# Kernel optimization log

Measured on AMD Instinct MI355X. Metric: run time of the kernel, lower is better.

The kernel has to match this reference:

```python
import jax, jax.numpy as jnp
import numpy as np

MASKING_RATIO = 0.5
EPS = 1e-6

def setup_inputs() -> dict:
    key = jax.random.key(0)
    x = jax.random.normal(key, (64, 256, 56, 56), dtype=jnp.float32)
    return {"x": x}

def reference(x):
    B, C, H, W = x.shape
    x_flat = x.reshape(B, C, H * W)
    # stable softmax over spatial dim, + eps as in the original
    probs = jax.nn.softmax(x_flat, axis=-1) + EPS
    entropy = -jnp.sum(probs * jnp.log(probs), axis=-1)  # [B, C]
    importance = -entropy
    k = int(C * (1.0 - MASKING_RATIO))
    _, topk_idx = jax.lax.top_k(importance, k)  # [B, k]
    mask = jnp.zeros((B, C), dtype=x.dtype)
    mask = mask.at[jnp.arange(B)[:, None], topk_idx].set(1.0)
    return x * mask[:, :, None, None]
```

## Files before the change

### kernel.cpp

```cpp
#include <hip/hip_runtime.h>
#include <math.h>

constexpr int BB   = 64;
constexpr int CC   = 256;
constexpr int HW   = 3136;
constexpr int NV4  = HW / 4;
constexpr int KSEL = 128;
#define EPSF 1e-6f

__device__ __forceinline__ float waveMax(float v) {
#pragma unroll
    for (int o = 32; o > 0; o >>= 1) v = fmaxf(v, __shfl_xor(v, o));
    return v;
}
__device__ __forceinline__ float waveSum(float v) {
#pragma unroll
    for (int o = 32; o > 0; o >>= 1) v += __shfl_xor(v, o);
    return v;
}
__device__ __forceinline__ int waveSumI(int v) {
#pragma unroll
    for (int o = 32; o > 0; o >>= 1) v += __shfl_xor(v, o);
    return v;
}

__global__ __launch_bounds__(256) void ent_kernel(const float* __restrict__ x,
                                                  float* __restrict__ ent) {
    __shared__ float red[4];
    const int row = blockIdx.x;
    const float4* __restrict__ xr =
        reinterpret_cast<const float4*>(x) + (size_t)row * NV4;
    const int t = threadIdx.x;

    float4 v[4];
    float lmax = -INFINITY;
#pragma unroll
    for (int j = 0; j < 4; ++j) {
        int idx = t + j * 256;
        if (idx < NV4) {
            v[j] = xr[idx];
            lmax = fmaxf(lmax, fmaxf(fmaxf(v[j].x, v[j].y), fmaxf(v[j].z, v[j].w)));
        }
    }
    float wm = waveMax(lmax);
    if ((t & 63) == 0) red[t >> 6] = wm;
    __syncthreads();
    const float m = fmaxf(fmaxf(red[0], red[1]), fmaxf(red[2], red[3]));
    __syncthreads();

    float4 e[4];
    float lsum = 0.f;
#pragma unroll
    for (int j = 0; j < 4; ++j) {
        int idx = t + j * 256;
        if (idx < NV4) {
            e[j].x = expf(v[j].x - m);
            e[j].y = expf(v[j].y - m);
            e[j].z = expf(v[j].z - m);
            e[j].w = expf(v[j].w - m);
            lsum += (e[j].x + e[j].y) + (e[j].z + e[j].w);
        }
    }
    float ws = waveSum(lsum);
    if ((t & 63) == 0) red[t >> 6] = ws;
    __syncthreads();
    const float S = (red[0] + red[1]) + (red[2] + red[3]);
    __syncthreads();
    const float invS = 1.0f / S;

    float lent = 0.f;
#pragma unroll
    for (int j = 0; j < 4; ++j) {
        int idx = t + j * 256;
        if (idx < NV4) {
            float p0 = e[j].x * invS + EPSF;
            float p1 = e[j].y * invS + EPSF;
            float p2 = e[j].z * invS + EPSF;
            float p3 = e[j].w * invS + EPSF;
            lent += p0 * logf(p0) + p1 * logf(p1) + p2 * logf(p2) + p3 * logf(p3);
        }
    }
    float we = waveSum(lent);
    if ((t & 63) == 0) red[t >> 6] = we;
    __syncthreads();
    if (t == 0) ent[row] = -((red[0] + red[1]) + (red[2] + red[3]));
}

__global__ __launch_bounds__(256) void apply_kernel(const float* __restrict__ x,
                                                    const float* __restrict__ ent,
                                                    float* __restrict__ out) {
    __shared__ int sred[4];
    __shared__ int skeep;
    const int row = blockIdx.x;
    const int b = row >> 8;
    const int c = row & (CC - 1);
    const int t = threadIdx.x;

    const float e_mine = ent[row];
    const float ej = ent[b * CC + t];
    int pred = (ej < e_mine) || (ej == e_mine && t < c);
    int wsum = waveSumI(pred);
    if ((t & 63) == 0) sred[t >> 6] = wsum;
    __syncthreads();
    if (t == 0) {
        int rank = (sred[0] + sred[1]) + (sred[2] + sred[3]);
        skeep = (rank < KSEL) ? 1 : 0;
    }
    __syncthreads();
    const int keep = skeep;

    const float4* __restrict__ xr =
        reinterpret_cast<const float4*>(x) + (size_t)row * NV4;
    float4* __restrict__ orow = reinterpret_cast<float4*>(out) + (size_t)row * NV4;
    if (keep) {
#pragma unroll
        for (int j = 0; j < 4; ++j) {
            int idx = t + j * 256;
            if (idx < NV4) orow[idx] = xr[idx];
        }
    } else {
        const float4 z = make_float4(0.f, 0.f, 0.f, 0.f);
#pragma unroll
        for (int j = 0; j < 4; ++j) {
            int idx = t + j * 256;
            if (idx < NV4) orow[idx] = z;
        }
    }
}

extern "C" void kernel_launch(void* const* d_in, const int* in_sizes, int n_in,
                              void* d_out, int out_size, void* d_ws, size_t ws_size,
                              hipStream_t stream) {
    const float* x = (const float*)d_in[0];
    float* out = (float*)d_out;
    float* ent = (float*)d_ws;

    ent_kernel<<<BB * CC, 256, 0, stream>>>(x, ent);
    apply_kernel<<<BB * CC, 256, 0, stream>>>(x, ent, out);
}
```

Before: 362.7 us.

## Compute entropy algebraically in one pass and use nontemporal output stores

The entropy kernel replaces the separate normalize-and-log pass with a closed-form expansion. Per thread it accumulates sum(e), sum(e*d), sum(d) and sum(1/e), then derives the entropy including a Taylor expansion of the eps term, which removes the per-element logf and one block reduction round. The apply kernel switches to nontemporal stores to keep output writes out of cache. The expansion changes numerics and the reciprocal of very small exponentials may overflow or lose accuracy, which could alter top-k ties.

```diff
diff --git a/kernel.cpp b/kernel.cpp
--- a/kernel.cpp
+++ b/kernel.cpp
@@ -7,6 +7,8 @@
 constexpr int NV4  = HW / 4;
 constexpr int KSEL = 128;
 #define EPSF 1e-6f
+
+typedef float vfloat4 __attribute__((ext_vector_type(4)));
 
 __device__ __forceinline__ float waveMax(float v) {
 #pragma unroll
@@ -26,13 +28,14 @@
 
 __global__ __launch_bounds__(256) void ent_kernel(const float* __restrict__ x,
                                                   float* __restrict__ ent) {
-    __shared__ float red[4];
+    __shared__ vfloat4 red4[4];
+    __shared__ float redm[4];
     const int row = blockIdx.x;
-    const float4* __restrict__ xr =
-        reinterpret_cast<const float4*>(x) + (size_t)row * NV4;
+    const vfloat4* __restrict__ xr =
+        reinterpret_cast<const vfloat4*>(x) + (size_t)row * NV4;
     const int t = threadIdx.x;
 
-    float4 v[4];
+    vfloat4 v[4];
     float lmax = -INFINITY;
 #pragma unroll
     for (int j = 0; j < 4; ++j) {
@@ -43,47 +46,41 @@
         }
     }
     float wm = waveMax(lmax);
-    if ((t & 63) == 0) red[t >> 6] = wm;
+    if ((t & 63) == 0) redm[t >> 6] = wm;
     __syncthreads();
-    const float m = fmaxf(fmaxf(red[0], red[1]), fmaxf(red[2], red[3]));
-    __syncthreads();
+    const float m = fmaxf(fmaxf(redm[0], redm[1]), fmaxf(redm[2], redm[3]));
 
-    float4 e[4];
-    float lsum = 0.f;
+    float S = 0.f, T = 0.f, U = 0.f, R = 0.f;
 #pragma unroll
     for (int j = 0; j < 4; ++j) {
         int idx = t + j * 256;
         if (idx < NV4) {
-            e[j].x = expf(v[j].x - m);
-            e[j].y = expf(v[j].y - m);
-            e[j].z = expf(v[j].z - m);
-            e[j].w = expf(v[j].w - m);
-            lsum += (e[j].x + e[j].y) + (e[j].z + e[j].w);
+            float d0 = v[j].x - m, d1 = v[j].y - m, d2 = v[j].z - m, d3 = v[j].w - m;
+            float e0 = expf(d0), e1 = expf(d1), e2 = expf(d2), e3 = expf(d3);
+            S += (e0 + e1) + (e2 + e3);
+            T = fmaf(e0, d0, T); T = fmaf(e1, d1, T);
+            T = fmaf(e2, d2, T); T = fmaf(e3, d3, T);
+            U += (d0 + d1) + (d2 + d3);
+            R += (__builtin_amdgcn_rcpf(e0) + __builtin_amdgcn_rcpf(e1)) +
+                 (__builtin_amdgcn_rcpf(e2) + __builtin_amdgcn_rcpf(e3));
         }
     }
-    float ws = waveSum(lsum);
-    if ((t & 63) == 0) red[t >> 6] = ws;
+    S = waveSum(S); T = waveSum(T); U = waveSum(U); R = waveSum(R);
+    if ((t & 63) == 0) { vfloat4 r = {S, T, U, R}; red4[t >> 6] = r; }
     __syncthreads();
-    const float S = (red[0] + red[1]) + (red[2] + red[3]);
-    __syncthreads();
-    const float invS = 1.0f / S;
-
-    float lent = 0.f;
-#pragma unroll
-    for (int j = 0; j < 4; ++j) {
-        int idx = t + j * 256;
-        if (idx < NV4) {
-            float p0 = e[j].x * invS + EPSF;
-            float p1 = e[j].y * invS + EPSF;
-            float p2 = e[j].z * invS + EPSF;
-            float p3 = e[j].w * invS + EPSF;
-            lent += p0 * logf(p0) + p1 * logf(p1) + p2 * logf(p2) + p3 * logf(p3);
-        }
+    if (t == 0) {
+        vfloat4 a = red4[0], b = red4[1], c = red4[2], d = red4[3];
+        float Sf = (a.x + b.x) + (c.x + d.x);
+        float Tf = (a.y + b.y) + (c.y + d.y);
+        float Uf = (a.z + b.z) + (c.z + d.z);
+        float Rf = (a.w + b.w) + (c.w + d.w);
+        float lnS = logf(Sf);
+        float negH = Tf / Sf - lnS
+                   + EPSF * (Uf - (float)HW * lnS)
+                   + (float)HW * EPSF
+                   + 0.5f * EPSF * EPSF * Sf * Rf;
+        ent[row] = -negH;
     }
-    float we = waveSum(lent);
-    if ((t & 63) == 0) red[t >> 6] = we;
-    __syncthreads();
-    if (t == 0) ent[row] = -((red[0] + red[1]) + (red[2] + red[3]));
 }
 
 __global__ __launch_bounds__(256) void apply_kernel(const float* __restrict__ x,
@@ -109,21 +106,21 @@
     __syncthreads();
     const int keep = skeep;
 
-    const float4* __restrict__ xr =
-        reinterpret_cast<const float4*>(x) + (size_t)row * NV4;
-    float4* __restrict__ orow = reinterpret_cast<float4*>(out) + (size_t)row * NV4;
+    const vfloat4* __restrict__ xr =
+        reinterpret_cast<const vfloat4*>(x) + (size_t)row * NV4;
+    vfloat4* __restrict__ orow = reinterpret_cast<vfloat4*>(out) + (size_t)row * NV4;
     if (keep) {
 #pragma unroll
         for (int j = 0; j < 4; ++j) {
             int idx = t + j * 256;
-            if (idx < NV4) orow[idx] = xr[idx];
+            if (idx < NV4) __builtin_nontemporal_store(xr[idx], &orow[idx]);
         }
     } else {
-        const float4 z = make_float4(0.f, 0.f, 0.f, 0.f);
+        const vfloat4 z = {0.f, 0.f, 0.f, 0.f};
 #pragma unroll
         for (int j = 0; j < 4; ++j) {
             int idx = t + j * 256;
-            if (idx < NV4) orow[idx] = z;
+            if (idx < NV4) __builtin_nontemporal_store(z, &orow[idx]);
         }
     }
 }
```

Result: faster. 347.4 us (-4.2%).
